# Optimization experiments

Hardware: AMD Instinct MI355X
Metric: run time of the kernel (lower is better)

## Reference

```python
import jax, jax.numpy as jnp
import numpy as np

N_CLASSES = 1000  # matches init_kwargs n_classes


def setup_inputs() -> dict:
    key = jax.random.key(0)
    k1, k2 = jax.random.split(key)
    N, D = 524288, 128
    embeddeds = jax.random.normal(k1, (N, D), dtype=jnp.float32)
    target = jax.random.randint(k2, (N,), 0, N_CLASSES, dtype=jnp.int32)
    return {"embeddeds": embeddeds, "target": target}


def reference(embeddeds, target):
    # Per-class counts and sums via segment reductions (replaces the Python loop
    # over classes with nonzero/gather/mean in the torch original).
    counts = jax.ops.segment_sum(
        jnp.ones(target.shape, dtype=embeddeds.dtype), target, num_segments=N_CLASSES
    )  # [C]
    sums = jax.ops.segment_sum(embeddeds, target, num_segments=N_CLASSES)  # [C, D]
    safe_counts = jnp.maximum(counts, 1.0)
    means = sums / safe_counts[:, None]  # [C, D], per-class mean embedding

    # Per-sample L2 distance to its class mean (mean_center=True branch).
    diffs = embeddeds - means[target]  # [N, D]
    norms = jnp.sqrt(jnp.sum(diffs * diffs, axis=1))  # [N]

    # Per-class mean of norms; empty classes contribute 0 (as in the torch code).
    per_class = jax.ops.segment_sum(norms, target, num_segments=N_CLASSES) / safe_counts
    per_class = jnp.where(counts > 0, per_class, 0.0)
    return jnp.sum(per_class)
```

## Files before the change

kernel.cpp:

```cpp
#include <hip/hip_runtime.h>
#include <hip/hip_bf16.h>

#define C 1000
#define D 128
#define PAD 16

__global__ __launch_bounds__(1024)
void k_hist(const int* __restrict__ tgt, unsigned* __restrict__ counts, int N) {
    __shared__ unsigned lh[C];
    const int t = threadIdx.x;
    if (t < C) lh[t] = 0u;
    __syncthreads();
    for (int i = blockIdx.x * 1024 + t; i < N; i += gridDim.x * 1024)
        atomicAdd(&lh[tgt[i]], 1u);
    __syncthreads();
    if (t < C) atomicAdd(&counts[t * PAD], lh[t]);
}

__global__ __launch_bounds__(1024)
void k_scan(const unsigned* __restrict__ counts, int* __restrict__ off,
            int* __restrict__ cursor) {
    __shared__ unsigned a[1024];
    const int t = threadIdx.x;
    const unsigned mine = (t < C) ? counts[t * PAD] : 0u;
    a[t] = mine;
    for (int o = 1; o < 1024; o <<= 1) {
        __syncthreads();
        const unsigned v = (t >= o) ? a[t - o] : 0u;
        __syncthreads();
        a[t] += v;
    }
    __syncthreads();
    if (t < C) {
        const unsigned excl = a[t] - mine;
        off[t] = (int)excl;
        cursor[t * PAD] = (int)excl;
    }
}

__global__ __launch_bounds__(256)
void k_scatter(const int* __restrict__ tgt, int* __restrict__ cursor,
               int* __restrict__ order, int N) {
    const int i = blockIdx.x * 256 + threadIdx.x;
    if (i >= N) return;
    const int c = tgt[i];
    const int pos = atomicAdd(&cursor[c * PAD], 1);
    order[pos] = i;
}

__global__ __launch_bounds__(512)
void k_fused(const float* __restrict__ emb, const int* __restrict__ order,
             const int* __restrict__ off, const unsigned* __restrict__ counts,
             float* __restrict__ percls) {
    __shared__ float part[8][D];
    __shared__ float mean_l[D];
    __shared__ float nacc[16];
    const int c    = blockIdx.x;
    const int t    = threadIdx.x;
    const int w    = t >> 6;
    const int lane = t & 63;
    const int half = lane >> 5;
    const int sub  = lane & 31;
    const int hw   = t >> 5;
    const int start = off[c];
    const int cnt   = (int)counts[c * PAD];

    const int chunk = (cnt + 7) >> 3;
    const int wsrt  = start + w * chunk;
    const int wend  = min(start + cnt, wsrt + chunk);
    float ax = 0.f, ay = 0.f, az = 0.f, aw = 0.f;
    for (int pos = wsrt + half; pos < wend; pos += 2) {
        const int ridx = order[pos];
        const float4 v = *reinterpret_cast<const float4*>(
            emb + (size_t)ridx * D + sub * 4);
        ax += v.x; ay += v.y; az += v.z; aw += v.w;
    }
    ax += __shfl_xor(ax, 32);
    ay += __shfl_xor(ay, 32);
    az += __shfl_xor(az, 32);
    aw += __shfl_xor(aw, 32);
    if (half == 0) {
        part[w][sub * 4 + 0] = ax;
        part[w][sub * 4 + 1] = ay;
        part[w][sub * 4 + 2] = az;
        part[w][sub * 4 + 3] = aw;
    }
    __syncthreads();
    if (t < D) {
        float s = 0.f;
        #pragma unroll
        for (int k = 0; k < 8; ++k) s += part[k][t];
        mean_l[t] = s / fmaxf((float)cnt, 1.f);
    }
    __syncthreads();

    const float4 m = *reinterpret_cast<const float4*>(mean_l + sub * 4);
    float local = 0.f;
    for (int pos = start + hw; pos < start + cnt; pos += 16) {
        const int ridx = order[pos];
        const float4 v = *reinterpret_cast<const float4*>(
            emb + (size_t)ridx * D + sub * 4);
        const float dx = v.x - m.x, dy = v.y - m.y, dz = v.z - m.z, dw = v.w - m.w;
        float p = dx * dx + dy * dy + dz * dz + dw * dw;
        p += __shfl_xor(p, 1);
        p += __shfl_xor(p, 2);
        p += __shfl_xor(p, 4);
        p += __shfl_xor(p, 8);
        p += __shfl_xor(p, 16);
        if (sub == 0) local += sqrtf(p);
    }
    if (sub == 0) nacc[hw] = local;
    __syncthreads();
    if (t == 0) {
        float tot = 0.f;
        #pragma unroll
        for (int k = 0; k < 16; ++k) tot += nacc[k];
        percls[c] = (cnt > 0) ? tot / (float)cnt : 0.f;
    }
}

__global__ __launch_bounds__(256)
void k_final(const float* __restrict__ percls, float* __restrict__ out) {
    __shared__ float red[256];
    float acc = 0.f;
    for (int c = threadIdx.x; c < C; c += 256) acc += percls[c];
    red[threadIdx.x] = acc;
    __syncthreads();
    for (int s = 128; s > 0; s >>= 1) {
        if (threadIdx.x < s) red[threadIdx.x] += red[threadIdx.x + s];
        __syncthreads();
    }
    if (threadIdx.x == 0) out[0] = red[0];
}

extern "C" void kernel_launch(void* const* d_in, const int* in_sizes, int n_in,
                              void* d_out, int out_size, void* d_ws, size_t ws_size,
                              hipStream_t stream) {
    const float* emb = (const float*)d_in[0];
    const int*   tgt = (const int*)d_in[1];
    const int N = in_sizes[1];

    char* ws = (char*)d_ws;
    unsigned* counts = (unsigned*)(ws);
    int*      off    = (int*)(ws + 65536);
    float*    percls = (float*)(ws + 73728);
    int*      cursor = (int*)(ws + 131072);
    int*      order  = (int*)(ws + 262144);

    hipMemsetAsync(d_ws, 0, 65536, stream);

    k_hist<<<256, 1024, 0, stream>>>(tgt, counts, N);
    k_scan<<<1, 1024, 0, stream>>>(counts, off, cursor);
    k_scatter<<<(N + 255) / 256, 256, 0, stream>>>(tgt, cursor, order, N);
    k_fused<<<C, 512, 0, stream>>>(emb, order, off, counts, percls);
    k_final<<<1, 256, 0, stream>>>(percls, (float*)d_out);
}
```

Measured before the change: 138.4 us.

## Unroll mean gather loop and stage rows in swizzled LDS for distance pass

The class-sum loop is unrolled eight rows deep so more independent gathers are in flight per wavefront. The distance pass now stages 64 gathered rows at a time into XOR-swizzled shared memory. Each row is then processed by 8 threads holding 16 floats each, which shortens the shuffle reduction from five steps to three. This adds 32KB of LDS per block and two barriers per chunk, which may lower occupancy. The rows are still re-read from global memory rather than reused from the first pass.

```diff
diff --git a/kernel.cpp b/kernel.cpp
--- a/kernel.cpp
+++ b/kernel.cpp
@@ -4,6 +4,9 @@
 #define C 1000
 #define D 128
 #define PAD 16
+#define CHUNK 64
+
+__device__ __forceinline__ void atomAddF(float* p, float v) { unsafeAtomicAdd(p, v); }
 
 __global__ __launch_bounds__(1024)
 void k_hist(const int* __restrict__ tgt, unsigned* __restrict__ counts, int N) {
@@ -54,7 +57,8 @@
              float* __restrict__ percls) {
     __shared__ float part[8][D];
     __shared__ float mean_l[D];
-    __shared__ float nacc[16];
+    __shared__ float stage[CHUNK * D];
+    __shared__ float nacc[8];
     const int c    = blockIdx.x;
     const int t    = threadIdx.x;
     const int w    = t >> 6;
@@ -65,15 +69,33 @@
     const int start = off[c];
     const int cnt   = (int)counts[c * PAD];
 
-    const int chunk = (cnt + 7) >> 3;
-    const int wsrt  = start + w * chunk;
-    const int wend  = min(start + cnt, wsrt + chunk);
+    const int chunkA = (cnt + 7) >> 3;
+    const int wsrt   = start + w * chunkA;
+    const int wend   = min(start + cnt, wsrt + chunkA);
     float ax = 0.f, ay = 0.f, az = 0.f, aw = 0.f;
-    for (int pos = wsrt + half; pos < wend; pos += 2) {
-        const int ridx = order[pos];
-        const float4 v = *reinterpret_cast<const float4*>(
-            emb + (size_t)ridx * D + sub * 4);
-        ax += v.x; ay += v.y; az += v.z; aw += v.w;
+    int pos = wsrt + half;
+    for (; pos + 14 < wend; pos += 16) {
+        const int r0 = order[pos];      const int r1 = order[pos + 2];
+        const int r2 = order[pos + 4];  const int r3 = order[pos + 6];
+        const int r4 = order[pos + 8];  const int r5 = order[pos + 10];
+        const int r6 = order[pos + 12]; const int r7 = order[pos + 14];
+        const float4 v0 = *reinterpret_cast<const float4*>(emb + (size_t)r0 * D + sub * 4);
+        const float4 v1 = *reinterpret_cast<const float4*>(emb + (size_t)r1 * D + sub * 4);
+        const float4 v2 = *reinterpret_cast<const float4*>(emb + (size_t)r2 * D + sub * 4);
+        const float4 v3 = *reinterpret_cast<const float4*>(emb + (size_t)r3 * D + sub * 4);
+        const float4 v4 = *reinterpret_cast<const float4*>(emb + (size_t)r4 * D + sub * 4);
+        const float4 v5 = *reinterpret_cast<const float4*>(emb + (size_t)r5 * D + sub * 4);
+        const float4 v6 = *reinterpret_cast<const float4*>(emb + (size_t)r6 * D + sub * 4);
+        const float4 v7 = *reinterpret_cast<const float4*>(emb + (size_t)r7 * D + sub * 4);
+        ax += (v0.x + v1.x) + (v2.x + v3.x) + (v4.x + v5.x) + (v6.x + v7.x);
+        ay += (v0.y + v1.y) + (v2.y + v3.y) + (v4.y + v5.y) + (v6.y + v7.y);
+        az += (v0.z + v1.z) + (v2.z + v3.z) + (v4.z + v5.z) + (v6.z + v7.z);
+        aw += (v0.w + v1.w) + (v2.w + v3.w) + (v4.w + v5.w) + (v6.w + v7.w);
+    }
+    for (; pos < wend; pos += 2) {
+        const int r0 = order[pos];
+        const float4 v0 = *reinterpret_cast<const float4*>(emb + (size_t)r0 * D + sub * 4);
+        ax += v0.x; ay += v0.y; az += v0.z; aw += v0.w;
     }
     ax += __shfl_xor(ax, 32);
     ay += __shfl_xor(ay, 32);
@@ -94,27 +116,63 @@
     }
     __syncthreads();
 
-    const float4 m = *reinterpret_cast<const float4*>(mean_l + sub * 4);
+    const int sub8 = t & 7;
+    const int rloc = t >> 3;
+    const float4 m0 = *reinterpret_cast<const float4*>(mean_l + (sub8 * 4 + 0) * 4);
+    const float4 m1 = *reinterpret_cast<const float4*>(mean_l + (sub8 * 4 + 1) * 4);
+    const float4 m2 = *reinterpret_cast<const float4*>(mean_l + (sub8 * 4 + 2) * 4);
+    const float4 m3 = *reinterpret_cast<const float4*>(mean_l + (sub8 * 4 + 3) * 4);
     float local = 0.f;
-    for (int pos = start + hw; pos < start + cnt; pos += 16) {
-        const int ridx = order[pos];
-        const float4 v = *reinterpret_cast<const float4*>(
-            emb + (size_t)ridx * D + sub * 4);
-        const float dx = v.x - m.x, dy = v.y - m.y, dz = v.z - m.z, dw = v.w - m.w;
-        float p = dx * dx + dy * dy + dz * dz + dw * dw;
-        p += __shfl_xor(p, 1);
-        p += __shfl_xor(p, 2);
-        p += __shfl_xor(p, 4);
-        p += __shfl_xor(p, 8);
-        p += __shfl_xor(p, 16);
-        if (sub == 0) local += sqrtf(p);
-    }
-    if (sub == 0) nacc[hw] = local;
+
+    for (int cb = 0; cb < cnt; cb += CHUNK) {
+        const int rem = min(CHUNK, cnt - cb);
+        {
+            const int lr = hw * 4;
+            const int q  = start + cb + lr;
+            float4 s0, s1, s2, s3;
+            if (lr + 0 < rem) s0 = *reinterpret_cast<const float4*>(emb + (size_t)order[q + 0] * D + sub * 4);
+            if (lr + 1 < rem) s1 = *reinterpret_cast<const float4*>(emb + (size_t)order[q + 1] * D + sub * 4);
+            if (lr + 2 < rem) s2 = *reinterpret_cast<const float4*>(emb + (size_t)order[q + 2] * D + sub * 4);
+            if (lr + 3 < rem) s3 = *reinterpret_cast<const float4*>(emb + (size_t)order[q + 3] * D + sub * 4);
+            if (lr + 0 < rem) *reinterpret_cast<float4*>(stage + (lr + 0) * D + ((sub ^ ((lr + 0) & 7)) << 2)) = s0;
+            if (lr + 1 < rem) *reinterpret_cast<float4*>(stage + (lr + 1) * D + ((sub ^ ((lr + 1) & 7)) << 2)) = s1;
+            if (lr + 2 < rem) *reinterpret_cast<float4*>(stage + (lr + 2) * D + ((sub ^ ((lr + 2) & 7)) << 2)) = s2;
+            if (lr + 3 < rem) *reinterpret_cast<float4*>(stage + (lr + 3) * D + ((sub ^ ((lr + 3) & 7)) << 2)) = s3;
+        }
+        __syncthreads();
+        if (rloc < rem) {
+            const float* srow = stage + rloc * D;
+            const int sw = rloc & 7;
+            const float4 x0 = *reinterpret_cast<const float4*>(srow + (((sub8 * 4 + 0) ^ sw) << 2));
+            const float4 x1 = *reinterpret_cast<const float4*>(srow + (((sub8 * 4 + 1) ^ sw) << 2));
+            const float4 x2 = *reinterpret_cast<const float4*>(srow + (((sub8 * 4 + 2) ^ sw) << 2));
+            const float4 x3 = *reinterpret_cast<const float4*>(srow + (((sub8 * 4 + 3) ^ sw) << 2));
+            float dx, dy, dz, dw;
+            dx = x0.x - m0.x; dy = x0.y - m0.y; dz = x0.z - m0.z; dw = x0.w - m0.w;
+            float p = dx * dx + dy * dy + dz * dz + dw * dw;
+            dx = x1.x - m1.x; dy = x1.y - m1.y; dz = x1.z - m1.z; dw = x1.w - m1.w;
+            p += dx * dx + dy * dy + dz * dz + dw * dw;
+            dx = x2.x - m2.x; dy = x2.y - m2.y; dz = x2.z - m2.z; dw = x2.w - m2.w;
+            p += dx * dx + dy * dy + dz * dz + dw * dw;
+            dx = x3.x - m3.x; dy = x3.y - m3.y; dz = x3.z - m3.z; dw = x3.w - m3.w;
+            p += dx * dx + dy * dy + dz * dz + dw * dw;
+            p += __shfl_xor(p, 1);
+            p += __shfl_xor(p, 2);
+            p += __shfl_xor(p, 4);
+            if (sub8 == 0) local += sqrtf(p);
+        }
+        __syncthreads();
+    }
+
+    local += __shfl_xor(local, 8);
+    local += __shfl_xor(local, 16);
+    local += __shfl_xor(local, 32);
+    if (lane == 0) nacc[w] = local;
     __syncthreads();
     if (t == 0) {
         float tot = 0.f;
         #pragma unroll
-        for (int k = 0; k < 16; ++k) tot += nacc[k];
+        for (int k = 0; k < 8; ++k) tot += nacc[k];
         percls[c] = (cnt > 0) ? tot / (float)cnt : 0.f;
     }
 }
```

Measured after the change: 151.0 us. 9.1% more time.
